# Performance work log

Hardware: AMD Instinct MI355X
Metric: run time of the kernel (lower is better)

The kernel has to match this reference:

```python
import jax, jax.numpy as jnp
import numpy as np

N_FEATURES = 1024
N_TOKENS = 65536


def _circulant(w):
    """C[i, j] = w[(j - i) mod n], matching torch circulant(tensor, 0).
    Example: w=[0,1,2] -> [[0,1,2],[2,0,1],[1,2,0]]."""
    n = w.shape[0]
    j = jnp.arange(n)[None, :]
    i = jnp.arange(n)[:, None]
    return w[(j - i) % n]  # [n, n]


def setup_inputs() -> dict:
    key = jax.random.key(0)
    kx, kw = jax.random.split(key)
    x = jax.random.normal(kx, (N_TOKENS, N_FEATURES), dtype=jnp.float32)
    # torch.rand -> uniform [0, 1)
    weight = jax.random.uniform(kw, (N_FEATURES,), dtype=jnp.float32)
    return {"x": x, "weight": weight}


def reference(x, weight):
    C = _circulant(weight)  # [n, n]
    # F.linear(x, C) = x @ C.T  ->  mm[b, i] = sum_j x[b, j] * C[i, j]
    mm_cx = jnp.einsum("bj,ij->bi", x, C)
    out = mm_cx * x + mm_cx + x
    return out
```

## Files before the change

### kernel.cpp

```cpp
#include <hip/hip_runtime.h>

typedef __attribute__((ext_vector_type(8))) _Float16 half8;
typedef __attribute__((ext_vector_type(4))) float f32x4;

#define NF       1024
#define BM       64
#define NTHREADS 512
#define NSLABS   8
#define SLABK    128
#define WCOPY0   2048
#define WCOPYS   2040
#define WTOT     (WCOPY0 + 7 * WCOPYS)

__global__ __launch_bounds__(NTHREADS, 2)
void circ_kernel(const float* __restrict__ x, const float* __restrict__ wsrc,
                 float* __restrict__ out) {
    __shared__ __align__(16) _Float16 lds_A[128 * 64 * 8];
    __shared__ __align__(16) _Float16 lds_W[WTOT];

    const int tid  = threadIdx.x;
    const int bm   = blockIdx.x;
    const int lane = tid & 63;
    const int wv   = tid >> 6;
    const int l15  = lane & 15;
    const int quad = lane >> 4;

    for (int idx = tid; idx < WTOT; idx += NTHREADS) {
        int s, t;
        if (idx < WCOPY0) { s = 0; t = idx; }
        else { int r = idx - WCOPY0; s = 1 + r / WCOPYS; t = r - (s - 1) * WCOPYS; }
        lds_W[idx] = (_Float16)wsrc[(t + s) & (NF - 1)];
    }

    const int sr  = tid >> 3;
    const int skc = tid & 7;
    const float* xrow = x + ((size_t)(bm * BM + sr) << 10) + skc * 16;

    f32x4 st[4];
    #pragma unroll
    for (int c = 0; c < 4; ++c) st[c] = *(const f32x4*)(xrow + c * 4);

    auto write_slab = [&](int slab) {
        half8 h0, h1;
        #pragma unroll
        for (int e = 0; e < 8; ++e) h0[e] = (_Float16)st[e >> 2][e & 3];
        #pragma unroll
        for (int e = 0; e < 8; ++e) h1[e] = (_Float16)st[2 + (e >> 2)][e & 3];
        int w0 = slab * 16 + skc * 2;
        *(half8*)&lds_A[(w0 * 64 + sr) * 8]       = h0;
        *(half8*)&lds_A[((w0 + 1) * 64 + sr) * 8] = h1;
    };
    write_slab(0);

    int bbase[8];
    #pragma unroll
    for (int f = 0; f < 8; ++f) {
        int icol = wv * 128 + f * 16 + l15;
        int o0   = 1024 + 8 * quad - icol;
        int s    = o0 & 7;
        int t0   = o0 - s;
        int offs = (s == 0) ? 0 : (WCOPY0 + (s - 1) * WCOPYS);
        bbase[f] = offs + t0;
    }

    f32x4 acc[4][8];
    #pragma unroll
    for (int a = 0; a < 4; ++a)
        #pragma unroll
        for (int b = 0; b < 8; ++b)
            acc[a][b] = (f32x4){0.f, 0.f, 0.f, 0.f};

    __syncthreads();

    for (int slab = 0; slab < NSLABS; ++slab) {
        if (slab + 1 < NSLABS) {
            const float* xs = xrow + (slab + 1) * SLABK;
            #pragma unroll
            for (int c = 0; c < 4; ++c) st[c] = *(const f32x4*)(xs + c * 4);
        }
        #pragma unroll
        for (int ks = 0; ks < 4; ++ks) {
            const int k0 = slab * SLABK + ks * 32;
            half8 bfr[8];
            #pragma unroll
            for (int f = 0; f < 8; ++f)
                bfr[f] = *(const half8*)&lds_W[bbase[f] + k0];
            half8 afr[4];
            #pragma unroll
            for (int mf = 0; mf < 4; ++mf)
                afr[mf] = *(const half8*)&lds_A[(((k0 >> 3) + quad) * 64 + mf * 16 + l15) * 8];
            #pragma unroll
            for (int mf = 0; mf < 4; ++mf)
                #pragma unroll
                for (int f = 0; f < 8; ++f)
                    acc[mf][f] = __builtin_amdgcn_mfma_f32_16x16x32_f16(
                        afr[mf], bfr[f], acc[mf][f], 0, 0, 0);
        }
        if (slab + 1 < NSLABS) write_slab(slab + 1);
        __syncthreads();
    }

    #pragma unroll
    for (int mf = 0; mf < 4; ++mf) {
        #pragma unroll
        for (int f = 0; f < 8; ++f) {
            int icol = wv * 128 + f * 16 + l15;
            f32x4 v = acc[mf][f];
            #pragma unroll
            for (int reg = 0; reg < 4; ++reg) {
                int m = mf * 16 + quad * 4 + reg;
                float xf = (float)lds_A[((icol >> 3) * 64 + m) * 8 + (icol & 7)];
                float mm = v[reg];
                out[((size_t)(bm * BM + m) << 10) + icol] = mm * xf + mm + xf;
            }
        }
    }
}

extern "C" void kernel_launch(void* const* d_in, const int* in_sizes, int n_in,
                              void* d_out, int out_size, void* d_ws, size_t ws_size,
                              hipStream_t stream) {
    const float* x = (const float*)d_in[0];
    const float* w = (const float*)d_in[1];
    float* o       = (float*)d_out;
    circ_kernel<<<dim3(65536 / BM), dim3(NTHREADS), 0, stream>>>(x, w, o);
}
```

Baseline: 484.6 us.

## Use 16 waves with 64-column tiles and reuse circulant B fragments across k-steps

The block grows to 1024 threads with 16 waves, each owning 64 output columns instead of 128, so the accumulator array shrinks from 32 to 16 tiles. The kernel also uses the circulant structure: B fragments for column tile f at step k equal those of tile f-2 at the previous step. Only two new B fragments are loaded from LDS per k-step, and the rest are rotated through a register ring. This cuts LDS read traffic and register pressure, but all 16 waves must still meet at the same per-slab barrier, and the x staging loads per thread are smaller.

```diff
diff --git a/kernel.cpp b/kernel.cpp
--- a/kernel.cpp
+++ b/kernel.cpp
@@ -5,14 +5,14 @@
 
 #define NF       1024
 #define BM       64
-#define NTHREADS 512
+#define NTHREADS 1024
 #define NSLABS   8
 #define SLABK    128
 #define WCOPY0   2048
 #define WCOPYS   2040
 #define WTOT     (WCOPY0 + 7 * WCOPYS)
 
-__global__ __launch_bounds__(NTHREADS, 2)
+__global__ __launch_bounds__(NTHREADS, 4)
 void circ_kernel(const float* __restrict__ x, const float* __restrict__ wsrc,
                  float* __restrict__ out) {
     __shared__ __align__(16) _Float16 lds_A[128 * 64 * 8];
@@ -32,79 +32,90 @@
         lds_W[idx] = (_Float16)wsrc[(t + s) & (NF - 1)];
     }
 
-    const int sr  = tid >> 3;
-    const int skc = tid & 7;
-    const float* xrow = x + ((size_t)(bm * BM + sr) << 10) + skc * 16;
+    const int sr  = tid >> 4;
+    const int skc = tid & 15;
+    const float* xrow = x + ((size_t)(bm * BM + sr) << 10) + skc * 8;
 
-    f32x4 st[4];
-    #pragma unroll
-    for (int c = 0; c < 4; ++c) st[c] = *(const f32x4*)(xrow + c * 4);
+    f32x4 st0 = *(const f32x4*)(xrow);
+    f32x4 st1 = *(const f32x4*)(xrow + 4);
 
     auto write_slab = [&](int slab) {
-        half8 h0, h1;
+        half8 h;
         #pragma unroll
-        for (int e = 0; e < 8; ++e) h0[e] = (_Float16)st[e >> 2][e & 3];
+        for (int e = 0; e < 4; ++e) h[e]     = (_Float16)st0[e];
         #pragma unroll
-        for (int e = 0; e < 8; ++e) h1[e] = (_Float16)st[2 + (e >> 2)][e & 3];
-        int w0 = slab * 16 + skc * 2;
-        *(half8*)&lds_A[(w0 * 64 + sr) * 8]       = h0;
-        *(half8*)&lds_A[((w0 + 1) * 64 + sr) * 8] = h1;
+        for (int e = 0; e < 4; ++e) h[4 + e] = (_Float16)st1[e];
+        int w = slab * 16 + skc;
+        *(half8*)&lds_A[(w * 64 + sr) * 8] = h;
     };
     write_slab(0);
 
-    int bbase[8];
-    #pragma unroll
-    for (int f = 0; f < 8; ++f) {
-        int icol = wv * 128 + f * 16 + l15;
+    int bbase0;
+    {
+        int icol = wv * 64 + l15;
         int o0   = 1024 + 8 * quad - icol;
         int s    = o0 & 7;
         int t0   = o0 - s;
         int offs = (s == 0) ? 0 : (WCOPY0 + (s - 1) * WCOPYS);
-        bbase[f] = offs + t0;
+        bbase0 = offs + t0;
     }
 
-    f32x4 acc[4][8];
+    f32x4 acc[4][4];
     #pragma unroll
     for (int a = 0; a < 4; ++a)
         #pragma unroll
-        for (int b = 0; b < 8; ++b)
+        for (int b = 0; b < 4; ++b)
             acc[a][b] = (f32x4){0.f, 0.f, 0.f, 0.f};
 
     __syncthreads();
 
+    half8 bfr[4];
+    #pragma unroll
+    for (int f = 0; f < 4; ++f)
+        bfr[f] = *(const half8*)&lds_W[bbase0 - 16 * f];
+
     for (int slab = 0; slab < NSLABS; ++slab) {
         if (slab + 1 < NSLABS) {
             const float* xs = xrow + (slab + 1) * SLABK;
-            #pragma unroll
-            for (int c = 0; c < 4; ++c) st[c] = *(const f32x4*)(xs + c * 4);
+            st0 = *(const f32x4*)(xs);
+            st1 = *(const f32x4*)(xs + 4);
         }
         #pragma unroll
         for (int ks = 0; ks < 4; ++ks) {
             const int k0 = slab * SLABK + ks * 32;
-            half8 bfr[8];
-            #pragma unroll
-            for (int f = 0; f < 8; ++f)
-                bfr[f] = *(const half8*)&lds_W[bbase[f] + k0];
             half8 afr[4];
             #pragma unroll
             for (int mf = 0; mf < 4; ++mf)
                 afr[mf] = *(const half8*)&lds_A[(((k0 >> 3) + quad) * 64 + mf * 16 + l15) * 8];
+            constexpr int ford[4] = {2, 3, 0, 1};
             #pragma unroll
             for (int mf = 0; mf < 4; ++mf)
                 #pragma unroll
-                for (int f = 0; f < 8; ++f)
+                for (int ff = 0; ff < 4; ++ff) {
+                    const int f = ford[ff];
                     acc[mf][f] = __builtin_amdgcn_mfma_f32_16x16x32_f16(
-                        afr[mf], bfr[f], acc[mf][f], 0, 0, 0);
+                        afr[mf], bfr[(f - 2 * ks) & 3], acc[mf][f], 0, 0, 0);
+                }
+            if (ks < 3) {
+                const int k0n = k0 + 32;
+                bfr[(0 - 2 * (ks + 1)) & 3] = *(const half8*)&lds_W[bbase0 + k0n];
+                bfr[(1 - 2 * (ks + 1)) & 3] = *(const half8*)&lds_W[bbase0 - 16 + k0n];
+            }
         }
-        if (slab + 1 < NSLABS) write_slab(slab + 1);
+        if (slab + 1 < NSLABS) {
+            const int k0n = (slab + 1) * SLABK;
+            bfr[0] = *(const half8*)&lds_W[bbase0 + k0n];
+            bfr[1] = *(const half8*)&lds_W[bbase0 - 16 + k0n];
+            write_slab(slab + 1);
+        }
         __syncthreads();
     }
 
     #pragma unroll
     for (int mf = 0; mf < 4; ++mf) {
         #pragma unroll
-        for (int f = 0; f < 8; ++f) {
-            int icol = wv * 128 + f * 16 + l15;
+        for (int f = 0; f < 4; ++f) {
+            int icol = wv * 64 + f * 16 + l15;
             f32x4 v = acc[mf][f];
             #pragma unroll
             for (int reg = 0; reg < 4; ++reg) {
```

Result: faster. 470.4 us (-2.9%).
